# Performance work log

Hardware: AMD Instinct MI355X
Metric: run time of the kernel (lower is better)

Reference implementation:

```python
import jax, jax.numpy as jnp
import numpy as np
from jax import lax


def _conv(x, w, b):
    # 3x3 conv, stride 1, padding 1 == SAME; NCHW / OIHW layout like torch
    y = lax.conv_general_dilated(x, w, window_strides=(1, 1), padding='SAME',
                                 dimension_numbers=('NCHW', 'OIHW', 'NCHW'))
    return y + b[None, :, None, None]


def _maxpool2(x):
    return lax.reduce_window(x, -jnp.inf, lax.max, (1, 1, 2, 2), (1, 1, 2, 2), 'VALID')


def _upsample2(x):
    # nearest-neighbor upsample, scale factor 2
    return jnp.repeat(jnp.repeat(x, 2, axis=2), 2, axis=3)


def setup_inputs() -> dict:
    key = jax.random.key(0)
    ks = jax.random.split(key, 10)
    B, H, W = 128, 128, 128
    n_codes, d = 512, 32
    s = 0.1
    return {
        'x': jax.random.normal(ks[0], (B, 1, H, W), jnp.float32),
        'w1': jax.random.normal(ks[1], (16, 1, 3, 3), jnp.float32) * s,
        'b1': jnp.zeros((16,), jnp.float32),
        'w2': jax.random.normal(ks[2], (32, 16, 3, 3), jnp.float32) * s,
        'b2': jnp.zeros((32,), jnp.float32),
        'codebook': jax.random.normal(ks[3], (n_codes, d), jnp.float32),
        'w3': jax.random.normal(ks[4], (16, 32, 3, 3), jnp.float32) * s,
        'b3': jnp.zeros((16,), jnp.float32),
        'w4': jax.random.normal(ks[5], (1, 16, 3, 3), jnp.float32) * s,
        'b4': jnp.zeros((1,), jnp.float32),
    }


def reference(x, w1, b1, w2, b2, codebook, w3, b3, w4, b4):
    # encoder
    h = jax.nn.gelu(_maxpool2(_conv(x, w1, b1)), approximate=False)
    h = _maxpool2(_conv(h, w2, b2))  # [B, 32, H/4, W/4]
    B, C, Hq, Wq = h.shape

    # VectorQuantize: euclidean nearest-code lookup on flattened fmap
    z = h.transpose(0, 2, 3, 1).reshape(B, Hq * Wq, C)  # [B, N, d]
    d2 = ((z * z).sum(-1, keepdims=True)
          - 2.0 * jnp.einsum('bnc,kc->bnk', z, codebook)
          + (codebook * codebook).sum(-1))  # [B, N, K]
    idx = jnp.argmin(d2, axis=-1)  # [B, N]
    quant = codebook[idx]  # [B, N, d]
    commit_loss = jnp.mean((lax.stop_gradient(quant) - z) ** 2)
    indices = idx.reshape(B, Hq, Wq)

    # decoder: NOTE the source discards the quantized output (x_flat) and
    # keeps feeding the pre-quantization fmap h forward; we match that.
    g = jax.nn.gelu(_conv(_upsample2(h), w3, b3), approximate=False)
    out = jnp.clip(_conv(_upsample2(g), w4, b4), -1.0, 1.0)
    return out, indices, commit_loss
```

## Files before the change

kernel.cpp:

```cpp
#include <hip/hip_runtime.h>
#include <math.h>

typedef float f32x2 __attribute__((ext_vector_type(2)));

__device__ __forceinline__ float gelu_f(float x) {
    return 0.5f * x * (1.0f + erff(x * 0.7071067811865476f));
}

__global__ __launch_bounds__(256) void kA(const float* __restrict__ x,
                                          const float* __restrict__ w1,
                                          const float* __restrict__ b1,
                                          float* __restrict__ h1,
                                          const float* __restrict__ cb,
                                          const float* __restrict__ w3,
                                          const float* __restrict__ w4,
                                          float* __restrict__ ccp,
                                          float* __restrict__ w3t,
                                          float* __restrict__ w4t,
                                          f32x2* __restrict__ w2d,
                                          const float* __restrict__ w2) {
    const int blk = blockIdx.x;
    const int t = threadIdx.x;
    if (blk >= 2048) {
        const int id = (blk - 2048) * 256 + t;
        {
            const float* row = cb + id * 32;
            float s = 0.f;
#pragma unroll
            for (int c = 0; c < 32; ++c) s += row[c] * row[c];
            ccp[id] = s;
        }
        {
            const float* w = w3 + id * 9;
            const float T00 = w[0], T01 = w[1], T02 = w[2];
            const float T10 = w[3] + w[6], T11 = w[4] + w[7], T12 = w[5] + w[8];
            const float T20 = w[0] + w[3], T21 = w[1] + w[4], T22 = w[2] + w[5];
            const float T30 = w[6], T31 = w[7], T32 = w[8];
            float* o = w3t + id * 16;
            o[0] = T00; o[1] = T00 + T01; o[2] = T01 + T02; o[3] = T02;
            o[4] = T10; o[5] = T10 + T11; o[6] = T11 + T12; o[7] = T12;
            o[8] = T20; o[9] = T20 + T21; o[10] = T21 + T22; o[11] = T22;
            o[12] = T30; o[13] = T30 + T31; o[14] = T31 + T32; o[15] = T32;
        }
        if (id < 16) {
            const float* w = w4 + id * 9;
            const float T00 = w[0], T01 = w[1], T02 = w[2];
            const float T10 = w[3] + w[6], T11 = w[4] + w[7], T12 = w[5] + w[8];
            const float T20 = w[0] + w[3], T21 = w[1] + w[4], T22 = w[2] + w[5];
            const float T30 = w[6], T31 = w[7], T32 = w[8];
            float* o = w4t + id * 16;
            o[0] = T00; o[1] = T00 + T01; o[2] = T01 + T02; o[3] = T02;
            o[4] = T10; o[5] = T10 + T11; o[6] = T11 + T12; o[7] = T12;
            o[8] = T20; o[9] = T20 + T21; o[10] = T21 + T22; o[11] = T22;
            o[12] = T30; o[13] = T30 + T31; o[14] = T31 + T32; o[15] = T32;
        }
        for (int i = id; i < 4608; i += 512) {
            const float wv = w2[i];
            w2d[i] = (f32x2){wv, wv};
        }
        return;
    }
    __shared__ float xs[34 * 38];
    const int b = blk >> 4;
    const int tile = blk & 15;
    const int ti = (tile >> 2) << 4, tj = (tile & 3) << 4;
    const float* xb = x + b * 16384;
    for (int i = t; i < 34 * 34; i += 256) {
        const int r = i / 34, c = i % 34;
        const int gr = 2 * ti - 1 + r, gc = 2 * tj - 1 + c;
        const float v = ((unsigned)gr < 128u && (unsigned)gc < 128u) ? xb[gr * 128 + gc] : 0.f;
        xs[r * 38 + (c & 1) * 19 + (c >> 1)] = v;
    }
    __syncthreads();
    const int jj = t & 15, ii = t >> 4;
    float pat[4][4];
#pragma unroll
    for (int r = 0; r < 4; r++) {
        const int row = (2 * ii + r) * 38;
        pat[r][0] = xs[row + jj];
        pat[r][1] = xs[row + 19 + jj];
        pat[r][2] = xs[row + jj + 1];
        pat[r][3] = xs[row + 20 + jj];
    }
    const int obase = b * 65536 + (ti + ii) * 64 + (tj + jj);
#pragma unroll 2
    for (int co = 0; co < 16; co++) {
        const float* wr = w1 + co * 9;
        float w[9];
#pragma unroll
        for (int k = 0; k < 9; k++) w[k] = wr[k];
        float s00 = 0.f, s01 = 0.f, s10 = 0.f, s11 = 0.f;
#pragma unroll
        for (int ty = 0; ty < 3; ty++)
#pragma unroll
            for (int tx = 0; tx < 3; tx++) {
                const float wv = w[ty * 3 + tx];
                s00 += wv * pat[ty][tx];
                s01 += wv * pat[ty][tx + 1];
                s10 += wv * pat[ty + 1][tx];
                s11 += wv * pat[ty + 1][tx + 1];
            }
        const float m = fmaxf(fmaxf(s00, s01), fmaxf(s10, s11)) + b1[co];
        h1[obase + co * 4096] = gelu_f(m);
    }
}

__global__ __launch_bounds__(256) void k_conv2(const float* __restrict__ h1,
                                               const f32x2* __restrict__ w2d,
                                               const float* __restrict__ b2,
                                               float* __restrict__ h) {
    __shared__ float hs[16 * 360];
    const int blk = blockIdx.x;
    const int b = blk >> 4;
    const int tile = blk & 15;
    const int ti = (tile >> 2) << 3, tj = (tile & 3) << 3;
    const int t = threadIdx.x;
    const float* h1b = h1 + b * 65536;
    for (int i = t; i < 16 * 324; i += 256) {
        const int ci = i / 324, rc = i % 324, r = rc / 18, c = rc % 18;
        const int gr = 2 * ti - 1 + r, gc = 2 * tj - 1 + c;
        const float v = ((unsigned)gr < 64u && (unsigned)gc < 64u) ? h1b[ci * 4096 + gr * 64 + gc] : 0.f;
        hs[ci * 360 + r * 20 + (c & 1) * 10 + (c >> 1)] = v;
    }
    __syncthreads();
    const int co0 = __builtin_amdgcn_readfirstlane((t >> 6) << 3);
    const int lane = t & 63;
    const int irow = lane >> 3, j = lane & 7;
    f32x2 A[8], B[8];
#pragma unroll
    for (int q = 0; q < 8; q++) { A[q] = (f32x2){0.f, 0.f}; B[q] = (f32x2){0.f, 0.f}; }
    const f32x2* wbase = w2d + co0 * 144;
#pragma unroll 4
    for (int ci = 0; ci < 16; ci++) {
        f32x2 P[4][3];
#pragma unroll
        for (int r = 0; r < 4; r++) {
            const int row = ci * 360 + (2 * irow + r) * 20;
            const float e0 = hs[row + j];
            const float o0 = hs[row + 10 + j];
            const float e1 = hs[row + j + 1];
            const float o1 = hs[row + 11 + j];
            P[r][0] = (f32x2){e0, o0};
            P[r][1] = (f32x2){o0, e1};
            P[r][2] = (f32x2){e1, o1};
        }
#pragma unroll
        for (int q = 0; q < 8; q++) {
            const f32x2* wr = wbase + q * 144 + ci * 9;
            f32x2 W[9];
#pragma unroll
            for (int k = 0; k < 9; k++) W[k] = wr[k];
#pragma unroll
            for (int ty = 0; ty < 3; ty++)
#pragma unroll
                for (int tx = 0; tx < 3; tx++) {
                    A[q] += P[ty][tx] * W[ty * 3 + tx];
                    B[q] += P[ty + 1][tx] * W[ty * 3 + tx];
                }
        }
    }
    float* hb = h + (b * 32 + co0) * 1024 + (ti + irow) * 32 + tj + j;
#pragma unroll
    for (int q = 0; q < 8; q++) {
        hb[q * 1024] = fmaxf(fmaxf(A[q].x, A[q].y), fmaxf(B[q].x, B[q].y)) + b2[co0 + q];
    }
}

__global__ __launch_bounds__(256) void kB(const float* __restrict__ h,
                                          const float* __restrict__ w3t,
                                          const float* __restrict__ b3,
                                          float* __restrict__ g,
                                          const float* __restrict__ cb,
                                          const float* __restrict__ ccp,
                                          float* __restrict__ idx_out,
                                          float* __restrict__ pa) {
    __shared__ float smem[16 * 350];
    const int blk = blockIdx.x;
    const int t = threadIdx.x;
    if (blk >= 512) {
        const int vblk = blk - 512;
        const int n0 = vblk * 64;
        const int wave = __builtin_amdgcn_readfirstlane(t >> 6);
        const int lane = t & 63;
        const int n = n0 + lane;
        const int b = n >> 10, pos = n & 1023;
        const float* hb = h + b * 32768 + pos;
        float z[32];
        float zz = 0.f;
#pragma unroll
        for (int c = 0; c < 32; ++c) {
            z[c] = hb[c * 1024];
            zz += z[c] * z[c];
        }
        f32x2 z2[16];
#pragma unroll
        for (int i = 0; i < 16; ++i) z2[i] = (f32x2){z[2 * i], z[2 * i + 1]};
        const int kbase = wave << 7;
        const float* cbb = cb + (kbase << 5);
        const float* ccb = ccp + kbase;
        float bd = 3.4e38f;
        int bk = 0;
#pragma unroll 1
        for (int kk = 0; kk < 128; kk += 2) {
            const f32x2* r0 = (const f32x2*)(cbb + (kk << 5));
            const f32x2* r1 = (const f32x2*)(cbb + (kk << 5) + 32);
            f32x2 D0 = (f32x2){0.f, 0.f};
            f32x2 D1 = (f32x2){0.f, 0.f};
#pragma unroll
            for (int i = 0; i < 16; ++i) {
                D0 += z2[i] * r0[i];
                D1 += z2[i] * r1[i];
            }
            const float dot0 = D0.x + D0.y;
            const float dot1 = D1.x + D1.y;
            const float e0 = (zz - 2.f * dot0) + ccb[kk];
            const float e1 = (zz - 2.f * dot1) + ccb[kk + 1];
            if (e0 < bd) { bd = e0; bk = kbase + kk; }
            if (e1 < bd) { bd = e1; bk = kbase + kk + 1; }
        }
        float2* sm = (float2*)smem;
        sm[wave * 64 + lane] = make_float2(bd, (float)bk);
        __syncthreads();
        if (t < 64) {
            float2 p0 = sm[t];
            float2 p1 = sm[64 + t];
            float2 p2 = sm[128 + t];
            float2 p3 = sm[192 + t];
            float fd = p0.x, fk = p0.y;
            if (p1.x < fd) { fd = p1.x; fk = p1.y; }
            if (p2.x < fd) { fd = p2.x; fk = p2.y; }
            if (p3.x < fd) { fd = p3.x; fk = p3.y; }
            idx_out[n0 + t] = fk;
            float s = fd;
#pragma unroll
            for (int m = 1; m < 64; m <<= 1) s += __shfl_xor(s, m, 64);
            if (t == 0) pa[vblk] = s;
        }
        return;
    }
    float* hS = smem;
    const int b = blk >> 2, strip = blk & 3;
    const int i0 = strip * 8;
    const int co0 = __builtin_amdgcn_readfirstlane((t >> 6) << 2);
    const int lane = t & 63;
    const int rp = lane >> 3, cg = lane & 7;
    float acc[4][2][8];
#pragma unroll
    for (int cq = 0; cq < 4; cq++)
#pragma unroll
        for (int rr = 0; rr < 2; rr++)
#pragma unroll
            for (int u = 0; u < 8; u++) acc[cq][rr][u] = 0.f;
    const float* hb = h + b * 32768;
#pragma unroll 1
    for (int chunk = 0; chunk < 2; chunk++) {
        __syncthreads();
        for (int i = t; i < 16 * 340; i += 256) {
            const int cil = i / 340, rc = i % 340, r = rc / 34, c = rc % 34;
            const int gr = i0 - 1 + r, gc = c - 1;
            const float v = ((unsigned)gr < 32u && (unsigned)gc < 32u)
                ? hb[(chunk * 16 + cil) * 1024 + gr * 32 + gc] : 0.f;
            hS[cil * 350 + r * 35 + c] = v;
        }
        __syncthreads();
#pragma unroll 2
        for (int cil = 0; cil < 16; cil++) {
            const int ci = chunk * 16 + cil;
            float colr[3][6];
#pragma unroll
            for (int rr = 0; rr < 3; rr++) {
                const int rowb = cil * 350 + (rp + rr) * 35 + 4 * cg;
#pragma unroll
                for (int u = 0; u < 6; u++) colr[rr][u] = hS[rowb + u];
            }
#pragma unroll
            for (int cq = 0; cq < 4; cq++) {
                const float* wt = w3t + ((co0 + cq) * 32 + ci) * 16;
                const float T00 = wt[0], O00 = wt[1], E01 = wt[2], T02 = wt[3];
                const float T10 = wt[4], O10 = wt[5], E11 = wt[6], T12 = wt[7];
                const float T20 = wt[8], O20 = wt[9], E21 = wt[10], T22 = wt[11];
                const float T30 = wt[12], O30 = wt[13], E31 = wt[14], T32 = wt[15];
#pragma unroll
                for (int mm = 0; mm < 4; mm++) {
                    acc[cq][0][2 * mm]     += T00 * colr[0][mm] + E01 * colr[0][mm + 1] + T10 * colr[1][mm] + E11 * colr[1][mm + 1];
                    acc[cq][0][2 * mm + 1] += O00 * colr[0][mm + 1] + T02 * colr[0][mm + 2] + O10 * colr[1][mm + 1] + T12 * colr[1][mm + 2];
                    acc[cq][1][2 * mm]     += T20 * colr[1][mm] + E21 * colr[1][mm + 1] + T30 * colr[2][mm] + E31 * colr[2][mm + 1];
                    acc[cq][1][2 * mm + 1] += O20 * colr[1][mm + 1] + T22 * colr[1][mm + 2] + O30 * colr[2][mm + 1] + T32 * colr[2][mm + 2];
                }
            }
        }
    }
    const int p_e = strip * 16 + 2 * rp;
#pragma unroll
    for (int cq = 0; cq < 4; cq++) {
        const float bias = b3[co0 + cq];
        float* gb = g + (b * 16 + co0 + cq) * 4096 + p_e * 64 + 8 * cg;
#pragma unroll
        for (int rr = 0; rr < 2; rr++) {
            float4 v0, v1;
            v0.x = gelu_f(acc[cq][rr][0] + bias);
            v0.y = gelu_f(acc[cq][rr][1] + bias);
            v0.z = gelu_f(acc[cq][rr][2] + bias);
            v0.w = gelu_f(acc[cq][rr][3] + bias);
            v1.x = gelu_f(acc[cq][rr][4] + bias);
            v1.y = gelu_f(acc[cq][rr][5] + bias);
            v1.z = gelu_f(acc[cq][rr][6] + bias);
            v1.w = gelu_f(acc[cq][rr][7] + bias);
            *(float4*)(gb + rr * 64) = v0;
            *(float4*)(gb + rr * 64 + 4) = v1;
        }
    }
}

__global__ __launch_bounds__(256) void kC(const float* __restrict__ g,
                                          const float* __restrict__ w4t,
                                          const float* __restrict__ b4,
                                          float* __restrict__ out,
                                          const float* __restrict__ pa,
                                          float* __restrict__ loss) {
    __shared__ float smem[8 * 690];
    const int blk = blockIdx.x;
    const int t = threadIdx.x;
    if (blk >= 1024) {
        float s = 0.f;
        for (int i = t; i < 2048; i += 256) s += pa[i];
        smem[t] = s;
        __syncthreads();
        for (int off = 128; off > 0; off >>= 1) {
            if (t < off) smem[t] += smem[t + off];
            __syncthreads();
        }
        if (t == 0) loss[0] = smem[0] * (1.0f / 4194304.0f);
        return;
    }
    float* gS = smem;
    const int b = blk >> 3, strip = blk & 7;
    const int i0 = strip * 8;
    const int rp = t >> 5, cg = t & 31;
    float acc[2][4];
#pragma unroll
    for (int rr = 0; rr < 2; rr++)
#pragma unroll
        for (int u = 0; u < 4; u++) acc[rr][u] = 0.f;
    const float* gbs = g + b * 65536;
#pragma unroll 1
    for (int chunk = 0; chunk < 2; chunk++) {
        __syncthreads();
        for (int i = t; i < 8 * 660; i += 256) {
            const int cil = i / 660, rc = i % 660, r = rc / 66, c = rc % 66;
            const int gr = i0 - 1 + r, gc = c - 1;
            const float v = ((unsigned)gr < 64u && (unsigned)gc < 64u)
                ? gbs[(chunk * 8 + cil) * 4096 + gr * 64 + gc] : 0.f;
            gS[cil * 690 + r * 69 + c] = v;
        }
        __syncthreads();
#pragma unroll 2
        for (int cil = 0; cil < 8; cil++) {
            const int ci = chunk * 8 + cil;
            float colv[3][4];
#pragma unroll
            for (int rr = 0; rr < 3; rr++) {
                const int rowb = cil * 690 + (rp + rr) * 69 + 2 * cg;
#pragma unroll
                for (int u = 0; u < 4; u++) colv[rr][u] = gS[rowb + u];
            }
            const float* wt = w4t + ci * 16;
            const float T00 = wt[0], O00 = wt[1], E01 = wt[2], T02 = wt[3];
            const float T10 = wt[4], O10 = wt[5], E11 = wt[6], T12 = wt[7];
            const float T20 = wt[8], O20 = wt[9], E21 = wt[10], T22 = wt[11];
            const float T30 = wt[12], O30 = wt[13], E31 = wt[14], T32 = wt[15];
#pragma unroll
            for (int mm = 0; mm < 2; mm++) {
                acc[0][2 * mm]     += T00 * colv[0][mm] + E01 * colv[0][mm + 1] + T10 * colv[1][mm] + E11 * colv[1][mm + 1];
                acc[0][2 * mm + 1] += O00 * colv[0][mm + 1] + T02 * colv[0][mm + 2] + O10 * colv[1][mm + 1] + T12 * colv[1][mm + 2];
                acc[1][2 * mm]     += T20 * colv[1][mm] + E21 * colv[1][mm + 1] + T30 * colv[2][mm] + E31 * colv[2][mm + 1];
                acc[1][2 * mm + 1] += O20 * colv[1][mm + 1] + T22 * colv[1][mm + 2] + O30 * colv[2][mm + 1] + T32 * colv[2][mm + 2];
            }
        }
    }
    const float bias = b4[0];
    const int p_e = strip * 16 + 2 * rp;
    float* ob = out + b * 16384 + p_e * 128 + 4 * cg;
#pragma unroll
    for (int rr = 0; rr < 2; rr++) {
        float4 v;
        v.x = fminf(fmaxf(acc[rr][0] + bias, -1.f), 1.f);
        v.y = fminf(fmaxf(acc[rr][1] + bias, -1.f), 1.f);
        v.z = fminf(fmaxf(acc[rr][2] + bias, -1.f), 1.f);
        v.w = fminf(fmaxf(acc[rr][3] + bias, -1.f), 1.f);
        *(float4*)(ob + rr * 128) = v;
    }
}

extern "C" void kernel_launch(void* const* d_in, const int* in_sizes, int n_in,
                              void* d_out, int out_size, void* d_ws, size_t ws_size,
                              hipStream_t stream) {
    const float* x  = (const float*)d_in[0];
    const float* w1 = (const float*)d_in[1];
    const float* b1 = (const float*)d_in[2];
    const float* w2 = (const float*)d_in[3];
    const float* b2 = (const float*)d_in[4];
    const float* cb = (const float*)d_in[5];
    const float* w3 = (const float*)d_in[6];
    const float* b3 = (const float*)d_in[7];
    const float* w4 = (const float*)d_in[8];
    const float* b4 = (const float*)d_in[9];

    float* ws = (float*)d_ws;
    float* h1 = ws;
    float* h  = ws + 8388608;
    float* g  = h1;
    float* ccp = ws + 12582912;
    float* pa  = ws + 12583424;
    float* w4t = ws + 12585472;

    float* outp = (float*)d_out;
    float* w3t = outp;
    f32x2* w2d = (f32x2*)(outp + 8192);
    float* idx = outp + 2097152;
    float* loss = outp + 2228224;

    kA<<<2050, 256, 0, stream>>>(x, w1, b1, h1, cb, w3, w4, ccp, w3t, w4t, w2d, w2);
    k_conv2<<<2048, 256, 0, stream>>>(h1, w2d, b2, h);
    kB<<<2560, 256, 0, stream>>>(h, w3t, b3, g, cb, ccp, idx, pa);
    kC<<<1025, 256, 0, stream>>>(g, w4t, b4, outp, pa, loss);
}
```

Baseline: 219.5 us.

## Stage VQ codebook in LDS with double-buffered DMA and merge conv2 tiles

The VQ part of kB is reorganised so each wave handles 64 distinct points over all 512 codes, rather than four waves splitting codes for the same 64 points. This removes the cross-wave argmin reduction through shared memory. The codebook is streamed into LDS in 64-code chunks using double-buffered global_load_lds, replacing repeated global loads, and VQ blocks are placed first in the grid. k_conv2 now has each block process two spatial tiles in sequence, halving the grid and amortising per-block setup. The risks are the extra barrier per chunk, the reliance on async LDS loads being complete at the barrier, and lower parallelism in conv2.

```diff
diff --git a/kernel.cpp b/kernel.cpp
--- a/kernel.cpp
+++ b/kernel.cpp
@@ -111,58 +111,63 @@
                                                float* __restrict__ h) {
     __shared__ float hs[16 * 360];
     const int blk = blockIdx.x;
-    const int b = blk >> 4;
-    const int tile = blk & 15;
-    const int ti = (tile >> 2) << 3, tj = (tile & 3) << 3;
+    const int b = blk >> 3;
+    const int tt = blk & 7;
     const int t = threadIdx.x;
-    const float* h1b = h1 + b * 65536;
-    for (int i = t; i < 16 * 324; i += 256) {
-        const int ci = i / 324, rc = i % 324, r = rc / 18, c = rc % 18;
-        const int gr = 2 * ti - 1 + r, gc = 2 * tj - 1 + c;
-        const float v = ((unsigned)gr < 64u && (unsigned)gc < 64u) ? h1b[ci * 4096 + gr * 64 + gc] : 0.f;
-        hs[ci * 360 + r * 20 + (c & 1) * 10 + (c >> 1)] = v;
-    }
-    __syncthreads();
     const int co0 = __builtin_amdgcn_readfirstlane((t >> 6) << 3);
     const int lane = t & 63;
     const int irow = lane >> 3, j = lane & 7;
-    f32x2 A[8], B[8];
-#pragma unroll
-    for (int q = 0; q < 8; q++) { A[q] = (f32x2){0.f, 0.f}; B[q] = (f32x2){0.f, 0.f}; }
+    const float* h1b = h1 + b * 65536;
     const f32x2* wbase = w2d + co0 * 144;
+#pragma unroll 1
+    for (int half = 0; half < 2; half++) {
+        const int tile = tt * 2 + half;
+        const int ti = (tile >> 2) << 3, tj = (tile & 3) << 3;
+        if (half) __syncthreads();
+        for (int i = t; i < 16 * 324; i += 256) {
+            const int ci = i / 324, rc = i % 324, r = rc / 18, c = rc % 18;
+            const int gr = 2 * ti - 1 + r, gc = 2 * tj - 1 + c;
+            const float v = ((unsigned)gr < 64u && (unsigned)gc < 64u) ? h1b[ci * 4096 + gr * 64 + gc] : 0.f;
+            hs[ci * 360 + r * 20 + (c & 1) * 10 + (c >> 1)] = v;
+        }
+        __syncthreads();
+        f32x2 A[8], B[8];
+#pragma unroll
+        for (int q = 0; q < 8; q++) { A[q] = (f32x2){0.f, 0.f}; B[q] = (f32x2){0.f, 0.f}; }
 #pragma unroll 4
-    for (int ci = 0; ci < 16; ci++) {
-        f32x2 P[4][3];
-#pragma unroll
-        for (int r = 0; r < 4; r++) {
-            const int row = ci * 360 + (2 * irow + r) * 20;
-            const float e0 = hs[row + j];
-            const float o0 = hs[row + 10 + j];
-            const float e1 = hs[row + j + 1];
-            const float o1 = hs[row + 11 + j];
-            P[r][0] = (f32x2){e0, o0};
-            P[r][1] = (f32x2){o0, e1};
-            P[r][2] = (f32x2){e1, o1};
-        }
+        for (int ci = 0; ci < 16; ci++) {
+            f32x2 P[4][3];
+#pragma unroll
+            for (int r = 0; r < 4; r++) {
+                const int row = ci * 360 + (2 * irow + r) * 20;
+                const float e0 = hs[row + j];
+                const float o0 = hs[row + 10 + j];
+                const float e1 = hs[row + j + 1];
+                const float o1 = hs[row + 11 + j];
+                P[r][0] = (f32x2){e0, o0};
+                P[r][1] = (f32x2){o0, e1};
+                P[r][2] = (f32x2){e1, o1};
+            }
+#pragma unroll
+            for (int q = 0; q < 8; q++) {
+                const f32x2* wr = wbase + q * 144 + ci * 9;
+                f32x2 W[9];
+#pragma unroll
+                for (int k = 0; k < 9; k++) W[k] = wr[k];
+#pragma unroll
+                for (int ty = 0; ty < 3; ty++)
+#pragma unroll
+                    for (int tx = 0; tx < 3; tx++) {
+                        A[q] += P[ty][tx] * W[ty * 3 + tx];
+                        B[q] += P[ty + 1][tx] * W[ty * 3 + tx];
+                    }
+            }
+        }
+        float* hb = h + (b * 32 + co0) * 1024 + (ti + irow) * 32 + tj + j;
 #pragma unroll
         for (int q = 0; q < 8; q++) {
-            const f32x2* wr = wbase + q * 144 + ci * 9;
-            f32x2 W[9];
-#pragma unroll
-            for (int k = 0; k < 9; k++) W[k] = wr[k];
-#pragma unroll
-            for (int ty = 0; ty < 3; ty++)
-#pragma unroll
-                for (int tx = 0; tx < 3; tx++) {
-                    A[q] += P[ty][tx] * W[ty * 3 + tx];
-                    B[q] += P[ty + 1][tx] * W[ty * 3 + tx];
-                }
-        }
-    }
-    float* hb = h + (b * 32 + co0) * 1024 + (ti + irow) * 32 + tj + j;
-#pragma unroll
-    for (int q = 0; q < 8; q++) {
-        hb[q * 1024] = fmaxf(fmaxf(A[q].x, A[q].y), fmaxf(B[q].x, B[q].y)) + b2[co0 + q];
+            hb[q * 1024] = fmaxf(fmaxf(A[q].x, A[q].y), fmaxf(B[q].x, B[q].y)) + b2[co0 + q];
+        }
     }
 }
 
@@ -177,13 +182,13 @@
     __shared__ float smem[16 * 350];
     const int blk = blockIdx.x;
     const int t = threadIdx.x;
-    if (blk >= 512) {
-        const int vblk = blk - 512;
-        const int n0 = vblk * 64;
-        const int wave = __builtin_amdgcn_readfirstlane(t >> 6);
+    if (blk < 512) {
+        const int vb = blk;
+        const int w = __builtin_amdgcn_readfirstlane(t >> 6);
         const int lane = t & 63;
-        const int n = n0 + lane;
-        const int b = n >> 10, pos = n & 1023;
+        const int n0 = vb * 256;
+        const int b = n0 >> 10;
+        const int pos = (n0 & 1023) + w * 64 + lane;
         const float* hb = h + b * 32768 + pos;
         float z[32];
         float zz = 0.f;
@@ -195,51 +200,64 @@
         f32x2 z2[16];
 #pragma unroll
         for (int i = 0; i < 16; ++i) z2[i] = (f32x2){z[2 * i], z[2 * i + 1]};
-        const int kbase = wave << 7;
-        const float* cbb = cb + (kbase << 5);
-        const float* ccb = ccp + kbase;
+        float* cbS = smem;
+#pragma unroll
+        for (int jj = 0; jj < 2; ++jj) {
+            const float* gsrc = cb + (w * 2 + jj) * 256 + lane * 4;
+            __builtin_amdgcn_global_load_lds(
+                (const __attribute__((address_space(1))) void*)gsrc,
+                (__attribute__((address_space(3))) void*)&cbS[(w * 2 + jj) * 256],
+                16, 0, 0);
+        }
+        __syncthreads();
         float bd = 3.4e38f;
         int bk = 0;
+        int buf = 0;
 #pragma unroll 1
-        for (int kk = 0; kk < 128; kk += 2) {
-            const f32x2* r0 = (const f32x2*)(cbb + (kk << 5));
-            const f32x2* r1 = (const f32x2*)(cbb + (kk << 5) + 32);
-            f32x2 D0 = (f32x2){0.f, 0.f};
-            f32x2 D1 = (f32x2){0.f, 0.f};
-#pragma unroll
-            for (int i = 0; i < 16; ++i) {
-                D0 += z2[i] * r0[i];
-                D1 += z2[i] * r1[i];
-            }
-            const float dot0 = D0.x + D0.y;
-            const float dot1 = D1.x + D1.y;
-            const float e0 = (zz - 2.f * dot0) + ccb[kk];
-            const float e1 = (zz - 2.f * dot1) + ccb[kk + 1];
-            if (e0 < bd) { bd = e0; bk = kbase + kk; }
-            if (e1 < bd) { bd = e1; bk = kbase + kk + 1; }
-        }
-        float2* sm = (float2*)smem;
-        sm[wave * 64 + lane] = make_float2(bd, (float)bk);
-        __syncthreads();
-        if (t < 64) {
-            float2 p0 = sm[t];
-            float2 p1 = sm[64 + t];
-            float2 p2 = sm[128 + t];
-            float2 p3 = sm[192 + t];
-            float fd = p0.x, fk = p0.y;
-            if (p1.x < fd) { fd = p1.x; fk = p1.y; }
-            if (p2.x < fd) { fd = p2.x; fk = p2.y; }
-            if (p3.x < fd) { fd = p3.x; fk = p3.y; }
-            idx_out[n0 + t] = fk;
-            float s = fd;
-#pragma unroll
-            for (int m = 1; m < 64; m <<= 1) s += __shfl_xor(s, m, 64);
-            if (t == 0) pa[vblk] = s;
-        }
+        for (int c = 0; c < 8; ++c) {
+            if (c < 7) {
+#pragma unroll
+                for (int jj = 0; jj < 2; ++jj) {
+                    const float* gsrc = cb + (c + 1) * 2048 + (w * 2 + jj) * 256 + lane * 4;
+                    __builtin_amdgcn_global_load_lds(
+                        (const __attribute__((address_space(1))) void*)gsrc,
+                        (__attribute__((address_space(3))) void*)&cbS[(buf ^ 1) * 2048 + (w * 2 + jj) * 256],
+                        16, 0, 0);
+                }
+            }
+            const float* base = &cbS[buf * 2048];
+#pragma unroll 4
+            for (int kk2 = 0; kk2 < 32; ++kk2) {
+                const int kk = c * 64 + kk2 * 2;
+                const f32x2* r0 = (const f32x2*)(base + kk2 * 64);
+                const f32x2* r1 = (const f32x2*)(base + kk2 * 64 + 32);
+                f32x2 D0 = (f32x2){0.f, 0.f};
+                f32x2 D1 = (f32x2){0.f, 0.f};
+#pragma unroll
+                for (int i = 0; i < 16; ++i) {
+                    D0 += z2[i] * r0[i];
+                    D1 += z2[i] * r1[i];
+                }
+                const float dot0 = D0.x + D0.y;
+                const float dot1 = D1.x + D1.y;
+                const float e0 = (zz - 2.f * dot0) + ccp[kk];
+                const float e1 = (zz - 2.f * dot1) + ccp[kk + 1];
+                if (e0 < bd) { bd = e0; bk = kk; }
+                if (e1 < bd) { bd = e1; bk = kk + 1; }
+            }
+            __syncthreads();
+            buf ^= 1;
+        }
+        idx_out[n0 + w * 64 + lane] = (float)bk;
+        float s = bd;
+#pragma unroll
+        for (int m = 1; m < 64; m <<= 1) s += __shfl_xor(s, m, 64);
+        if (lane == 0) pa[vb * 4 + w] = s;
         return;
     }
     float* hS = smem;
-    const int b = blk >> 2, strip = blk & 3;
+    const int cblk = blk - 512;
+    const int b = cblk >> 2, strip = cblk & 3;
     const int i0 = strip * 8;
     const int co0 = __builtin_amdgcn_readfirstlane((t >> 6) << 2);
     const int lane = t & 63;
@@ -421,7 +439,7 @@
     float* loss = outp + 2228224;
 
     kA<<<2050, 256, 0, stream>>>(x, w1, b1, h1, cb, w3, w4, ccp, w3t, w4t, w2d, w2);
-    k_conv2<<<2048, 256, 0, stream>>>(h1, w2d, b2, h);
-    kB<<<2560, 256, 0, stream>>>(h, w3t, b3, g, cb, ccp, idx, pa);
+    k_conv2<<<1024, 256, 0, stream>>>(h1, w2d, b2, h);
+    kB<<<1024, 256, 0, stream>>>(h, w3t, b3, g, cb, ccp, idx, pa);
     kC<<<1025, 256, 0, stream>>>(g, w4t, b4, outp, pa, loss);
 }
```

Result: no change. 219.6 us (+0.0%).

## Split VQ codebook search across blocks and merge with 64-bit atomicMin

Applied to the files above, without the earlier changes.

The VQ argmin no longer reduces four codebook slices across the waves of one block through shared memory. Each block now handles one codebook quarter for 256 points, with one point per lane, and merges results through a 64-bit atomicMin on an order-preserving (distance, index) key in global memory. A new small kernel decodes the keys into indices and per-block loss partial sums, and kA initializes the key buffer. This removes the block barrier and the idle waves during the final reduction and lets every wave in a block share one codebook slice. In exchange it adds global atomics, an extra kernel launch and a key-buffer initialization pass.

```diff
diff --git a/kernel.cpp b/kernel.cpp
--- a/kernel.cpp
+++ b/kernel.cpp
@@ -18,7 +18,8 @@
                                           float* __restrict__ w3t,
                                           float* __restrict__ w4t,
                                           f32x2* __restrict__ w2d,
-                                          const float* __restrict__ w2) {
+                                          const float* __restrict__ w2,
+                                          unsigned long long* __restrict__ minkey) {
     const int blk = blockIdx.x;
     const int t = threadIdx.x;
     if (blk >= 2048) {
@@ -58,6 +59,7 @@
             const float wv = w2[i];
             w2d[i] = (f32x2){wv, wv};
         }
+        for (int i = id; i < 131072; i += 512) minkey[i] = 0xFFFFFFFFFFFFFFFFull;
         return;
     }
     __shared__ float xs[34 * 38];
@@ -172,17 +174,17 @@
                                           float* __restrict__ g,
                                           const float* __restrict__ cb,
                                           const float* __restrict__ ccp,
-                                          float* __restrict__ idx_out,
-                                          float* __restrict__ pa) {
+                                          unsigned long long* __restrict__ minkey) {
     __shared__ float smem[16 * 350];
     const int blk = blockIdx.x;
     const int t = threadIdx.x;
     if (blk >= 512) {
         const int vblk = blk - 512;
-        const int n0 = vblk * 64;
+        const int ks = vblk >> 9;
+        const int nc = vblk & 511;
         const int wave = __builtin_amdgcn_readfirstlane(t >> 6);
         const int lane = t & 63;
-        const int n = n0 + lane;
+        const int n = nc * 256 + wave * 64 + lane;
         const int b = n >> 10, pos = n & 1023;
         const float* hb = h + b * 32768 + pos;
         float z[32];
@@ -195,7 +197,7 @@
         f32x2 z2[16];
 #pragma unroll
         for (int i = 0; i < 16; ++i) z2[i] = (f32x2){z[2 * i], z[2 * i + 1]};
-        const int kbase = wave << 7;
+        const int kbase = ks << 7;
         const float* cbb = cb + (kbase << 5);
         const float* ccb = ccp + kbase;
         float bd = 3.4e38f;
@@ -218,24 +220,10 @@
             if (e0 < bd) { bd = e0; bk = kbase + kk; }
             if (e1 < bd) { bd = e1; bk = kbase + kk + 1; }
         }
-        float2* sm = (float2*)smem;
-        sm[wave * 64 + lane] = make_float2(bd, (float)bk);
-        __syncthreads();
-        if (t < 64) {
-            float2 p0 = sm[t];
-            float2 p1 = sm[64 + t];
-            float2 p2 = sm[128 + t];
-            float2 p3 = sm[192 + t];
-            float fd = p0.x, fk = p0.y;
-            if (p1.x < fd) { fd = p1.x; fk = p1.y; }
-            if (p2.x < fd) { fd = p2.x; fk = p2.y; }
-            if (p3.x < fd) { fd = p3.x; fk = p3.y; }
-            idx_out[n0 + t] = fk;
-            float s = fd;
-#pragma unroll
-            for (int m = 1; m < 64; m <<= 1) s += __shfl_xor(s, m, 64);
-            if (t == 0) pa[vblk] = s;
-        }
+        const unsigned u = __float_as_uint(bd);
+        const unsigned m = (u & 0x80000000u) ? ~u : (u | 0x80000000u);
+        const unsigned long long key = (((unsigned long long)m) << 32) | (unsigned)bk;
+        atomicMin(&minkey[n], key);
         return;
     }
     float* hS = smem;
@@ -312,6 +300,31 @@
     }
 }
 
+__global__ __launch_bounds__(256) void k_ext(const unsigned long long* __restrict__ minkey,
+                                             float* __restrict__ idx_out,
+                                             float* __restrict__ pa) {
+    __shared__ float red[256];
+    const int t = threadIdx.x;
+    const int base = blockIdx.x * 2048;
+    float s = 0.f;
+#pragma unroll
+    for (int i = 0; i < 8; ++i) {
+        const int n = base + i * 256 + t;
+        const unsigned long long key = minkey[n];
+        idx_out[n] = (float)(unsigned)(key & 0xFFFFFFFFu);
+        const unsigned m = (unsigned)(key >> 32);
+        const unsigned u = (m & 0x80000000u) ? (m ^ 0x80000000u) : ~m;
+        s += __uint_as_float(u);
+    }
+    red[t] = s;
+    __syncthreads();
+    for (int off = 128; off > 0; off >>= 1) {
+        if (t < off) red[t] += red[t + off];
+        __syncthreads();
+    }
+    if (t == 0) pa[blockIdx.x] = red[0];
+}
+
 __global__ __launch_bounds__(256) void kC(const float* __restrict__ g,
                                           const float* __restrict__ w4t,
                                           const float* __restrict__ b4,
@@ -322,8 +335,7 @@
     const int blk = blockIdx.x;
     const int t = threadIdx.x;
     if (blk >= 1024) {
-        float s = 0.f;
-        for (int i = t; i < 2048; i += 256) s += pa[i];
+        float s = (t < 64) ? pa[t] : 0.f;
         smem[t] = s;
         __syncthreads();
         for (int off = 128; off > 0; off >>= 1) {
@@ -412,7 +424,8 @@
     float* g  = h1;
     float* ccp = ws + 12582912;
     float* pa  = ws + 12583424;
-    float* w4t = ws + 12585472;
+    float* w4t = ws + 12583552;
+    unsigned long long* minkey = (unsigned long long*)(ws + 12583936);
 
     float* outp = (float*)d_out;
     float* w3t = outp;
@@ -420,8 +433,9 @@
     float* idx = outp + 2097152;
     float* loss = outp + 2228224;
 
-    kA<<<2050, 256, 0, stream>>>(x, w1, b1, h1, cb, w3, w4, ccp, w3t, w4t, w2d, w2);
+    kA<<<2050, 256, 0, stream>>>(x, w1, b1, h1, cb, w3, w4, ccp, w3t, w4t, w2d, w2, minkey);
     k_conv2<<<2048, 256, 0, stream>>>(h1, w2d, b2, h);
-    kB<<<2560, 256, 0, stream>>>(h, w3t, b3, g, cb, ccp, idx, pa);
+    kB<<<2560, 256, 0, stream>>>(h, w3t, b3, g, cb, ccp, minkey);
+    k_ext<<<64, 256, 0, stream>>>(minkey, idx, pa);
     kC<<<1025, 256, 0, stream>>>(g, w4t, b4, outp, pa, loss);
 }
```

Result: slower. 241.6 us (+10.1%).
